# Performance work log

Measured on AMD Instinct MI355X. Metric: run time of the kernel, lower is better.

The kernel has to match this reference:

```python
import jax, jax.numpy as jnp
import numpy as np

DIN = 1024
DIM = 1024
NUM_HEADS = 16
HEAD_DIM = DIM // NUM_HEADS
SEQ_LEN = 2048
BATCH = 2


def setup_inputs() -> dict:
    key = jax.random.key(0)
    ks = jax.random.split(key, 5)
    s = 0.02
    x = jax.random.normal(ks[0], (BATCH, SEQ_LEN, DIN), dtype=jnp.float32)
    # torch nn.Linear weights are (out_features, in_features)
    wq = jax.random.normal(ks[1], (DIM, DIN), dtype=jnp.float32) * s
    wk = jax.random.normal(ks[2], (DIM, DIN), dtype=jnp.float32) * s
    wv = jax.random.normal(ks[3], (DIM, DIN), dtype=jnp.float32) * s
    wo = jax.random.normal(ks[4], (DIM, DIM), dtype=jnp.float32) * s
    return {"x": x, "wq": wq, "wk": wk, "wv": wv, "wo": wo}


def reference(x, wq, wk, wv, wo):
    bs, seq_len, _ = x.shape
    # project and split heads: [b, h, s, d]
    def split(z):
        return z.reshape(bs, seq_len, NUM_HEADS, HEAD_DIM).transpose(0, 2, 1, 3)
    q = split(x @ wq.T)
    k = split(x @ wk.T)
    v = split(x @ wv.T)
    # raw scores, causal mask applied BEFORE the 1/sqrt(d) scaling (as in source;
    # -inf is invariant to positive scaling so math matches standard causal attn)
    att = jnp.einsum('bhqd,bhkd->bhqk', q, k)
    causal = jnp.triu(jnp.ones((seq_len, seq_len), dtype=bool), k=1)
    att = jnp.where(causal, -jnp.inf, att)
    att = jax.nn.softmax(att / jnp.sqrt(jnp.float32(HEAD_DIM)), axis=-1)
    ctx = jnp.einsum('bhqk,bhkd->bhqd', att, v)
    ctx = ctx.transpose(0, 2, 1, 3).reshape(bs, seq_len, DIM)
    return ctx @ wo.T
```

## Files before the change

kernel.cpp:

```cpp
#include <hip/hip_runtime.h>
#include <stdint.h>

#define DIN 1024
#define DIMM 1024
#define NH 16
#define HD 64
#define SEQ 2048
#define BATCH 2
#define MTOT (BATCH*SEQ)
#define SCALE 0.125f

typedef __bf16 bf16;
typedef __bf16 bf16x8 __attribute__((ext_vector_type(8)));
typedef __bf16 bf16x4 __attribute__((ext_vector_type(4)));
typedef float f32x4 __attribute__((ext_vector_type(4)));

__device__ __forceinline__ void async16(bf16* lds, const bf16* g) {
  __builtin_amdgcn_global_load_lds(
      (const __attribute__((address_space(1))) void*)g,
      (__attribute__((address_space(3))) void*)lds, 16, 0, 0);
}

#define WAIT_VM(n)  asm volatile("s_waitcnt vmcnt(" #n ")" ::: "memory")
#define BARRIER()   asm volatile("s_barrier" ::: "memory")

__global__ __launch_bounds__(256) void convert_all(const float* __restrict__ x,
                                                   const float* __restrict__ wq,
                                                   const float* __restrict__ wk,
                                                   const float* __restrict__ wv,
                                                   const float* __restrict__ wo,
                                                   bf16* __restrict__ xb,
                                                   bf16* __restrict__ Wb) {
  const int t = blockIdx.x * 256 + threadIdx.x;
#pragma unroll
  for (int i = 0; i < 4; ++i) {
    const int c = t + i * 262144;
    const float* src;
    bf16* dst;
    if (c < 524288) {
      src = x + (size_t)c * 8;
      dst = xb + (size_t)c * 8;
    } else {
      const int cw = c - 524288;
      const int w = cw >> 17;
      const int off = (cw & 131071) * 8;
      const float* wp = (w == 0) ? wq : (w == 1) ? wk : (w == 2) ? wv : wo;
      src = wp + off;
      dst = Wb + (size_t)w * 1048576 + off;
    }
    f32x4 a = *(const f32x4*)src;
    f32x4 b = *(const f32x4*)(src + 4);
    bf16x8 r;
    r[0] = (bf16)a[0]; r[1] = (bf16)a[1]; r[2] = (bf16)a[2]; r[3] = (bf16)a[3];
    r[4] = (bf16)b[0]; r[5] = (bf16)b[1]; r[6] = (bf16)b[2]; r[7] = (bf16)b[3];
    *(bf16x8*)dst = r;
  }
}

__global__ __launch_bounds__(256, 2) void qkv_gemm(const bf16* __restrict__ A,
                                                   const bf16* __restrict__ B,
                                                   bf16* __restrict__ Q,
                                                   bf16* __restrict__ Kb,
                                                   bf16* __restrict__ Vt) {
  __shared__ bf16 As0[128 * 64];
  __shared__ bf16 As1[128 * 64];
  __shared__ bf16 Bs0[192 * 64];
  __shared__ bf16 Bs1[192 * 64];
  const int tid  = threadIdx.x;
  const int lane = tid & 63;
  const int wave = tid >> 6;
  const int lrow = lane & 15;
  const int quad = lane >> 4;
  const int wrow = wave >> 1;
  const int wcol = wave & 1;
  const int lin  = blockIdx.x;
  const int xcd  = lin & 7;
  const int idx  = lin >> 3;
  const int nbase = (xcd * 2 + (idx & 1)) * 192;
  const int mbase = (idx >> 1) * 128;

  const int srow = tid >> 3;
  const int sdst = srow * 64 + (tid & 7) * 8;
  const int sx   = ((tid & 7) ^ (srow & 7)) * 8;

  const bf16* ap = A + (size_t)(mbase + srow) * DIN + sx;
  const bf16* bp = B + (size_t)(nbase + srow) * DIN + sx;

  f32x4 acc[4][6] = {};

#define QKV_STAGE(Asb, Bsb)                                          \
  do {                                                               \
    _Pragma("unroll")                                                \
    for (int i = 0; i < 4; ++i)                                      \
      async16(&Asb[sdst + i * 2048], ap + (size_t)i * 32 * DIN);     \
    _Pragma("unroll")                                                \
    for (int i = 0; i < 6; ++i)                                      \
      async16(&Bsb[sdst + i * 2048], bp + (size_t)i * 32 * DIN);     \
  } while (0)

#define QKV_COMPUTE(Asb, Bsb)                                        \
  do {                                                               \
    __builtin_amdgcn_s_setprio(1);                                   \
    _Pragma("unroll")                                                \
    for (int h = 0; h < 2; ++h) {                                    \
      const int cx = ((h * 4 + quad) ^ (lrow & 7)) * 8;              \
      bf16x8 af[4], bfr[6];                                          \
      _Pragma("unroll")                                              \
      for (int i = 0; i < 4; ++i)                                    \
        af[i] = *(const bf16x8*)&Asb[(wrow * 64 + i * 16 + lrow) * 64 + cx]; \
      _Pragma("unroll")                                              \
      for (int j = 0; j < 6; ++j)                                    \
        bfr[j] = *(const bf16x8*)&Bsb[(wcol * 96 + j * 16 + lrow) * 64 + cx]; \
      _Pragma("unroll")                                              \
      for (int i = 0; i < 4; ++i)                                    \
        _Pragma("unroll")                                            \
        for (int j = 0; j < 6; ++j)                                  \
          acc[i][j] = __builtin_amdgcn_mfma_f32_16x16x32_bf16(af[i], bfr[j], acc[i][j], 0, 0, 0); \
    }                                                                \
    __builtin_amdgcn_s_setprio(0);                                   \
  } while (0)

  QKV_STAGE(As0, Bs0);
  WAIT_VM(0);
  BARRIER();

#pragma unroll 1
  for (int t = 0; t < 16; t += 2) {
    ap += 64; bp += 64;
    QKV_STAGE(As1, Bs1);
    WAIT_VM(10);
    BARRIER();
    QKV_COMPUTE(As0, Bs0);
    BARRIER();
    if (t + 2 < 16) {
      ap += 64; bp += 64;
      QKV_STAGE(As0, Bs0);
      WAIT_VM(10);
    } else {
      WAIT_VM(0);
    }
    BARRIER();
    QKV_COMPUTE(As1, Bs1);
    BARRIER();
  }

#undef QKV_STAGE
#undef QKV_COMPUTE

  const float C1 = 0.18033688f;
#pragma unroll
  for (int mt = 0; mt < 4; ++mt) {
    const int m0 = mbase + wrow * 64 + mt * 16 + quad * 4;
#pragma unroll
    for (int nt = 0; nt < 6; ++nt) {
      const int n16 = nbase + wcol * 96 + nt * 16;
      const int n = n16 + lrow;
      if (n16 < 1024) {
#pragma unroll
        for (int rr = 0; rr < 4; ++rr)
          Q[(size_t)(m0 + rr) * 1024 + n] = (bf16)(acc[mt][nt][rr] * C1);
      } else if (n16 < 2048) {
#pragma unroll
        for (int rr = 0; rr < 4; ++rr)
          Kb[(size_t)(m0 + rr) * 1024 + (n - 1024)] = (bf16)acc[mt][nt][rr];
      } else {
        const int nn = n - 2048;
        const int row = ((m0 >> 11) * 16 + (nn >> 6)) * 64 + (nn & 63);
        const int kb  = m0 & 2047;
        const int colp = (kb & ~31) | (quad * 8) | ((mt & 1) * 4);
        bf16x4 ov;
#pragma unroll
        for (int rr = 0; rr < 4; ++rr) ov[rr] = (bf16)acc[mt][nt][rr];
        *(bf16x4*)&Vt[(size_t)row * SEQ + colp] = ov;
      }
    }
  }
}

__global__ __launch_bounds__(256, 2) void proj_gemm(const bf16* __restrict__ A,
                                                    const bf16* __restrict__ B,
                                                    float* __restrict__ C) {
  __shared__ bf16 As0[128 * 64];
  __shared__ bf16 As1[128 * 64];
  __shared__ bf16 Bs0[64 * 64];
  __shared__ bf16 Bs1[64 * 64];
  const int tid  = threadIdx.x;
  const int lane = tid & 63;
  const int wave = tid >> 6;
  const int lrow = lane & 15;
  const int quad = lane >> 4;
  const int wr = (wave >> 1) * 64;
  const int wc = (wave & 1) * 32;
  const int lin = blockIdx.x;
  const int xcd = lin & 7;
  const int idx = lin >> 3;
  const int nbase = (xcd * 2 + (idx & 1)) * 64;
  const int mbase = (idx >> 1) * 128;
  const int srow = tid >> 3;
  const int sdst = srow * 64 + (tid & 7) * 8;
  const int sx   = ((tid & 7) ^ (srow & 7)) * 8;

  const bf16* ap = A + (size_t)(mbase + srow) * DIMM + sx;
  const bf16* bp = B + (size_t)(nbase + srow) * DIMM + sx;

  f32x4 acc[4][2] = {};

#define PRJ_STAGE(Asb, Bsb)                                          \
  do {                                                               \
    _Pragma("unroll")                                                \
    for (int i = 0; i < 4; ++i)                                      \
      async16(&Asb[sdst + i * 2048], ap + (size_t)i * 32 * DIMM);    \
    _Pragma("unroll")                                                \
    for (int i = 0; i < 2; ++i)                                      \
      async16(&Bsb[sdst + i * 2048], bp + (size_t)i * 32 * DIMM);    \
  } while (0)

#define PRJ_COMPUTE(Asb, Bsb)                                        \
  do {                                                               \
    __builtin_amdgcn_s_setprio(1);                                   \
    _Pragma("unroll")                                                \
    for (int h = 0; h < 2; ++h) {                                    \
      const int cx = ((h * 4 + quad) ^ (lrow & 7)) * 8;              \
      bf16x8 af[4], bfr[2];                                          \
      _Pragma("unroll")                                              \
      for (int i = 0; i < 4; ++i)                                    \
        af[i] = *(const bf16x8*)&Asb[(wr + i * 16 + lrow) * 64 + cx]; \
      _Pragma("unroll")                                              \
      for (int i = 0; i < 2; ++i)                                    \
        bfr[i] = *(const bf16x8*)&Bsb[(wc + i * 16 + lrow) * 64 + cx]; \
      _Pragma("unroll")                                              \
      for (int mt = 0; mt < 4; ++mt)                                 \
        _Pragma("unroll")                                            \
        for (int nt = 0; nt < 2; ++nt)                               \
          acc[mt][nt] = __builtin_amdgcn_mfma_f32_16x16x32_bf16(af[mt], bfr[nt], acc[mt][nt], 0, 0, 0); \
    }                                                                \
    __builtin_amdgcn_s_setprio(0);                                   \
  } while (0)

  PRJ_STAGE(As0, Bs0);
  WAIT_VM(0);
  BARRIER();

#pragma unroll 1
  for (int t = 0; t < 16; t += 2) {
    ap += 64; bp += 64;
    PRJ_STAGE(As1, Bs1);
    WAIT_VM(6);
    BARRIER();
    PRJ_COMPUTE(As0, Bs0);
    BARRIER();
    if (t + 2 < 16) {
      ap += 64; bp += 64;
      PRJ_STAGE(As0, Bs0);
      WAIT_VM(6);
    } else {
      WAIT_VM(0);
    }
    BARRIER();
    PRJ_COMPUTE(As1, Bs1);
    BARRIER();
  }

#undef PRJ_STAGE
#undef PRJ_COMPUTE

#pragma unroll
  for (int mt = 0; mt < 4; ++mt) {
    const int m0 = mbase + wr + mt * 16 + quad * 4;
#pragma unroll
    for (int nt = 0; nt < 2; ++nt) {
      const int n = nbase + wc + nt * 16 + lrow;
#pragma unroll
      for (int rr = 0; rr < 4; ++rr)
        C[(size_t)(m0 + rr) * 1024 + n] = acc[mt][nt][rr];
    }
  }
}

__global__ __launch_bounds__(256, 2) void attn(const bf16* __restrict__ Q,
                                               const bf16* __restrict__ K,
                                               const bf16* __restrict__ Vt,
                                               bf16* __restrict__ O) {
  __shared__ bf16 Ks[2][128 * 64];
  __shared__ bf16 Vts[2][128 * 64];
  const int tid  = threadIdx.x;
  const int wave = tid >> 6;
  const int lane = tid & 63;
  const int lrow = lane & 15;
  const int quad = lane >> 4;
  const int lin  = blockIdx.x;
  const int bh   = lin & 31;
  const int pp   = lin >> 5;
  const int b = bh >> 4;
  const int h = bh & 15;

  const bf16* Qh  = Q  + (size_t)(b * SEQ) * DIMM + h * HD;
  const bf16* Kh  = K  + (size_t)(b * SEQ) * DIMM + h * HD;
  const bf16* Vth = Vt + (size_t)bh * 64 * SEQ;

  const int srow = tid >> 3;
  const int sdst = srow * 64 + (tid & 7) * 8;
  const int sx   = ((tid & 7) ^ (srow & 7)) * 8;
  const int cx0 = ((0 + quad) ^ (lrow & 7)) * 8;
  const int cx1 = ((4 + quad) ^ (lrow & 7)) * 8;

#define ATT_STAGE(buf, kg, vg)                                        \
  do {                                                                \
    _Pragma("unroll")                                                 \
    for (int i = 0; i < 4; ++i)                                       \
      async16(&Ks[buf][sdst + i * 2048], kg + (size_t)i * 32 * DIMM); \
    async16(&Vts[buf][sdst],        vg);                              \
    async16(&Vts[buf][sdst + 2048], vg + (size_t)32 * SEQ);           \
    async16(&Vts[buf][sdst + 4096], vg + 64);                         \
    async16(&Vts[buf][sdst + 6144], vg + (size_t)32 * SEQ + 64);      \
  } while (0)

#pragma unroll 1
  for (int seg = 0; seg < 2; ++seg) {
    const int qi = seg ? pp : (31 - pp);
    const int qw = qi * 64 + wave * 16;
    const int nt = (qi + 2) >> 1;

    bf16x8 qf0 = *(const bf16x8*)&Qh[(size_t)(qw + lrow) * DIMM + quad * 8];
    bf16x8 qf1 = *(const bf16x8*)&Qh[(size_t)(qw + lrow) * DIMM + 32 + quad * 8];

    const bf16* kg = Kh + (size_t)srow * DIMM + sx;
    const bf16* vg = Vth + (size_t)srow * SEQ + sx;

    ATT_STAGE(0, kg, vg);
    __syncthreads();

    f32x4 lacc = {};
    f32x4 o_acc[4] = {};
    int cur = 0;

    for (int kt = 0; kt < nt; ++kt) {
      if (kt + 1 < nt) {
        kg += 128 * DIMM; vg += 128;
        const int nb = cur ^ 1;
        ATT_STAGE(nb, kg, vg);
      }
      const bf16* Kc = Ks[cur];
      const bf16* Vc = Vts[cur];
      f32x4 s[8];
#pragma unroll
      for (int gg = 0; gg < 8; ++gg) {
        s[gg] = f32x4{};
        bf16x8 kf0 = *(const bf16x8*)&Kc[(gg * 16 + lrow) * 64 + cx0];
        bf16x8 kf1 = *(const bf16x8*)&Kc[(gg * 16 + lrow) * 64 + cx1];
        s[gg] = __builtin_amdgcn_mfma_f32_16x16x32_bf16(kf0, qf0, s[gg], 0, 0, 0);
        s[gg] = __builtin_amdgcn_mfma_f32_16x16x32_bf16(kf1, qf1, s[gg], 0, 0, 0);
      }
      if (kt == nt - 1) {
        const int qrow = qw + lrow;
        const int kbase = kt * 128;
#pragma unroll
        for (int gg = 0; gg < 8; ++gg)
#pragma unroll
          for (int r = 0; r < 4; ++r)
            s[gg][r] = (kbase + gg * 16 + quad * 4 + r > qrow) ? -1e30f : s[gg][r];
      }
      bf16x8 pf0, pf1, pf2, pf3;
#pragma unroll
      for (int gg = 0; gg < 8; ++gg)
#pragma unroll
        for (int r = 0; r < 4; ++r) {
          const float p = __builtin_amdgcn_exp2f(s[gg][r]);
          lacc[r] += p;
          if      (gg < 2) pf0[(gg & 1) * 4 + r] = (bf16)p;
          else if (gg < 4) pf1[(gg & 1) * 4 + r] = (bf16)p;
          else if (gg < 6) pf2[(gg & 1) * 4 + r] = (bf16)p;
          else             pf3[(gg & 1) * 4 + r] = (bf16)p;
        }
#pragma unroll
      for (int dt = 0; dt < 4; ++dt) {
        const bf16* Vr0 = &Vc[(dt * 16 + lrow) * 64];
        const bf16* Vr1 = &Vc[4096 + (dt * 16 + lrow) * 64];
        bf16x8 vA = *(const bf16x8*)&Vr0[cx0];
        bf16x8 vB = *(const bf16x8*)&Vr0[cx1];
        bf16x8 vC = *(const bf16x8*)&Vr1[cx0];
        bf16x8 vD = *(const bf16x8*)&Vr1[cx1];
        o_acc[dt] = __builtin_amdgcn_mfma_f32_16x16x32_bf16(vA, pf0, o_acc[dt], 0, 0, 0);
        o_acc[dt] = __builtin_amdgcn_mfma_f32_16x16x32_bf16(vB, pf1, o_acc[dt], 0, 0, 0);
        o_acc[dt] = __builtin_amdgcn_mfma_f32_16x16x32_bf16(vC, pf2, o_acc[dt], 0, 0, 0);
        o_acc[dt] = __builtin_amdgcn_mfma_f32_16x16x32_bf16(vD, pf3, o_acc[dt], 0, 0, 0);
      }
      __syncthreads();
      cur ^= 1;
    }

    float lsum = (lacc[0] + lacc[1]) + (lacc[2] + lacc[3]);
    lsum += __shfl_xor(lsum, 16);
    lsum += __shfl_xor(lsum, 32);
    const float rl = __builtin_amdgcn_rcpf(lsum);
    bf16* Ob = O + (size_t)(b * SEQ + qw + lrow) * DIMM + h * HD;
#pragma unroll
    for (int dt = 0; dt < 4; ++dt) {
      bf16x4 ov;
#pragma unroll
      for (int r = 0; r < 4; ++r)
        ov[r] = (bf16)(o_acc[dt][r] * rl);
      *(bf16x4*)&Ob[dt * 16 + quad * 4] = ov;
    }
  }
#undef ATT_STAGE
}

extern "C" void kernel_launch(void* const* d_in, const int* in_sizes, int n_in,
                              void* d_out, int out_size, void* d_ws, size_t ws_size,
                              hipStream_t stream) {
  const float* x  = (const float*)d_in[0];
  const float* wq = (const float*)d_in[1];
  const float* wk = (const float*)d_in[2];
  const float* wv = (const float*)d_in[3];
  const float* wo = (const float*)d_in[4];

  const size_t M4 = (size_t)MTOT * DIMM;
  bf16* xb  = (bf16*)d_ws;
  bf16* Wb  = xb + M4;
  bf16* Q   = Wb + M4;
  bf16* Kb  = Q + M4;
  bf16* Vt  = Kb + M4;
  bf16* CTX = xb;
  float* out = (float*)d_out;

  convert_all<<<dim3(1024), dim3(256), 0, stream>>>(x, wq, wk, wv, wo, xb, Wb);
  qkv_gemm<<<dim3(512), dim3(256), 0, stream>>>(xb, Wb, Q, Kb, Vt);
  attn<<<dim3(512), dim3(256), 0, stream>>>(Q, Kb, Vt, CTX);
  proj_gemm<<<dim3(512), dim3(256), 0, stream>>>(CTX, Wb + 3 * 1048576, out);
}
```

Before: 157.6 us.

## Double attention query tile per block so each wave processes two query sub-tiles

The attention kernel now gives each block a 128-row query tile, with each wave handling two 16-row sub-tiles. Every K/V tile staged in LDS is therefore reused across twice as many queries, halving K/V global traffic and LDS fragment loads per query row. Grid size halves to 256 blocks and launch bounds drop to one block per CU to make room for the doubled registers. The risk is lower occupancy, fewer blocks than a GPU with many CUs can keep busy, and coarser causal load balancing across blocks.

```diff
diff --git a/kernel.cpp b/kernel.cpp
--- a/kernel.cpp
+++ b/kernel.cpp
@@ -277,7 +277,7 @@
   }
 }
 
-__global__ __launch_bounds__(256, 2) void attn(const bf16* __restrict__ Q,
+__global__ __launch_bounds__(256, 1) void attn(const bf16* __restrict__ Q,
                                                const bf16* __restrict__ K,
                                                const bf16* __restrict__ Vt,
                                                bf16* __restrict__ O) {
@@ -317,12 +317,14 @@
 
 #pragma unroll 1
   for (int seg = 0; seg < 2; ++seg) {
-    const int qi = seg ? pp : (31 - pp);
-    const int qw = qi * 64 + wave * 16;
-    const int nt = (qi + 2) >> 1;
-
-    bf16x8 qf0 = *(const bf16x8*)&Qh[(size_t)(qw + lrow) * DIMM + quad * 8];
-    bf16x8 qf1 = *(const bf16x8*)&Qh[(size_t)(qw + lrow) * DIMM + 32 + quad * 8];
+    const int qi = seg ? pp : (15 - pp);
+    const int qbw = qi * 128 + wave * 32;
+    const int nt = qi + 1;
+
+    bf16x8 qf0a = *(const bf16x8*)&Qh[(size_t)(qbw + lrow) * DIMM + quad * 8];
+    bf16x8 qf1a = *(const bf16x8*)&Qh[(size_t)(qbw + lrow) * DIMM + 32 + quad * 8];
+    bf16x8 qf0b = *(const bf16x8*)&Qh[(size_t)(qbw + 16 + lrow) * DIMM + quad * 8];
+    bf16x8 qf1b = *(const bf16x8*)&Qh[(size_t)(qbw + 16 + lrow) * DIMM + 32 + quad * 8];
 
     const bf16* kg = Kh + (size_t)srow * DIMM + sx;
     const bf16* vg = Vth + (size_t)srow * SEQ + sx;
@@ -330,47 +332,54 @@
     ATT_STAGE(0, kg, vg);
     __syncthreads();
 
-    f32x4 lacc = {};
-    f32x4 o_acc[4] = {};
+    f32x4 lacca = {}, laccb = {};
+    f32x4 oa[4] = {}, ob[4] = {};
     int cur = 0;
 
     for (int kt = 0; kt < nt; ++kt) {
       if (kt + 1 < nt) {
         kg += 128 * DIMM; vg += 128;
-        const int nb = cur ^ 1;
-        ATT_STAGE(nb, kg, vg);
+        ATT_STAGE(cur ^ 1, kg, vg);
       }
       const bf16* Kc = Ks[cur];
       const bf16* Vc = Vts[cur];
-      f32x4 s[8];
+      f32x4 sa[8], sb[8];
 #pragma unroll
       for (int gg = 0; gg < 8; ++gg) {
-        s[gg] = f32x4{};
+        sa[gg] = f32x4{}; sb[gg] = f32x4{};
         bf16x8 kf0 = *(const bf16x8*)&Kc[(gg * 16 + lrow) * 64 + cx0];
         bf16x8 kf1 = *(const bf16x8*)&Kc[(gg * 16 + lrow) * 64 + cx1];
-        s[gg] = __builtin_amdgcn_mfma_f32_16x16x32_bf16(kf0, qf0, s[gg], 0, 0, 0);
-        s[gg] = __builtin_amdgcn_mfma_f32_16x16x32_bf16(kf1, qf1, s[gg], 0, 0, 0);
+        sa[gg] = __builtin_amdgcn_mfma_f32_16x16x32_bf16(kf0, qf0a, sa[gg], 0, 0, 0);
+        sa[gg] = __builtin_amdgcn_mfma_f32_16x16x32_bf16(kf1, qf1a, sa[gg], 0, 0, 0);
+        sb[gg] = __builtin_amdgcn_mfma_f32_16x16x32_bf16(kf0, qf0b, sb[gg], 0, 0, 0);
+        sb[gg] = __builtin_amdgcn_mfma_f32_16x16x32_bf16(kf1, qf1b, sb[gg], 0, 0, 0);
       }
       if (kt == nt - 1) {
-        const int qrow = qw + lrow;
         const int kbase = kt * 128;
+        const int qra = qbw + lrow;
+        const int qrb = qbw + 16 + lrow;
 #pragma unroll
         for (int gg = 0; gg < 8; ++gg)
 #pragma unroll
-          for (int r = 0; r < 4; ++r)
-            s[gg][r] = (kbase + gg * 16 + quad * 4 + r > qrow) ? -1e30f : s[gg][r];
-      }
-      bf16x8 pf0, pf1, pf2, pf3;
+          for (int r = 0; r < 4; ++r) {
+            const int kk = kbase + gg * 16 + quad * 4 + r;
+            sa[gg][r] = (kk > qra) ? -1e30f : sa[gg][r];
+            sb[gg][r] = (kk > qrb) ? -1e30f : sb[gg][r];
+          }
+      }
+      bf16x8 pfa0, pfa1, pfa2, pfa3, pfb0, pfb1, pfb2, pfb3;
 #pragma unroll
       for (int gg = 0; gg < 8; ++gg)
 #pragma unroll
         for (int r = 0; r < 4; ++r) {
-          const float p = __builtin_amdgcn_exp2f(s[gg][r]);
-          lacc[r] += p;
-          if      (gg < 2) pf0[(gg & 1) * 4 + r] = (bf16)p;
-          else if (gg < 4) pf1[(gg & 1) * 4 + r] = (bf16)p;
-          else if (gg < 6) pf2[(gg & 1) * 4 + r] = (bf16)p;
-          else             pf3[(gg & 1) * 4 + r] = (bf16)p;
+          const float pa = __builtin_amdgcn_exp2f(sa[gg][r]);
+          const float pb = __builtin_amdgcn_exp2f(sb[gg][r]);
+          lacca[r] += pa;
+          laccb[r] += pb;
+          if      (gg < 2) { pfa0[(gg & 1) * 4 + r] = (bf16)pa; pfb0[(gg & 1) * 4 + r] = (bf16)pb; }
+          else if (gg < 4) { pfa1[(gg & 1) * 4 + r] = (bf16)pa; pfb1[(gg & 1) * 4 + r] = (bf16)pb; }
+          else if (gg < 6) { pfa2[(gg & 1) * 4 + r] = (bf16)pa; pfb2[(gg & 1) * 4 + r] = (bf16)pb; }
+          else             { pfa3[(gg & 1) * 4 + r] = (bf16)pa; pfb3[(gg & 1) * 4 + r] = (bf16)pb; }
         }
 #pragma unroll
       for (int dt = 0; dt < 4; ++dt) {
@@ -380,27 +389,39 @@
         bf16x8 vB = *(const bf16x8*)&Vr0[cx1];
         bf16x8 vC = *(const bf16x8*)&Vr1[cx0];
         bf16x8 vD = *(const bf16x8*)&Vr1[cx1];
-        o_acc[dt] = __builtin_amdgcn_mfma_f32_16x16x32_bf16(vA, pf0, o_acc[dt], 0, 0, 0);
-        o_acc[dt] = __builtin_amdgcn_mfma_f32_16x16x32_bf16(vB, pf1, o_acc[dt], 0, 0, 0);
-        o_acc[dt] = __builtin_amdgcn_mfma_f32_16x16x32_bf16(vC, pf2, o_acc[dt], 0, 0, 0);
-        o_acc[dt] = __builtin_amdgcn_mfma_f32_16x16x32_bf16(vD, pf3, o_acc[dt], 0, 0, 0);
+        oa[dt] = __builtin_amdgcn_mfma_f32_16x16x32_bf16(vA, pfa0, oa[dt], 0, 0, 0);
+        oa[dt] = __builtin_amdgcn_mfma_f32_16x16x32_bf16(vB, pfa1, oa[dt], 0, 0, 0);
+        oa[dt] = __builtin_amdgcn_mfma_f32_16x16x32_bf16(vC, pfa2, oa[dt], 0, 0, 0);
+        oa[dt] = __builtin_amdgcn_mfma_f32_16x16x32_bf16(vD, pfa3, oa[dt], 0, 0, 0);
+        ob[dt] = __builtin_amdgcn_mfma_f32_16x16x32_bf16(vA, pfb0, ob[dt], 0, 0, 0);
+        ob[dt] = __builtin_amdgcn_mfma_f32_16x16x32_bf16(vB, pfb1, ob[dt], 0, 0, 0);
+        ob[dt] = __builtin_amdgcn_mfma_f32_16x16x32_bf16(vC, pfb2, ob[dt], 0, 0, 0);
+        ob[dt] = __builtin_amdgcn_mfma_f32_16x16x32_bf16(vD, pfb3, ob[dt], 0, 0, 0);
       }
       __syncthreads();
       cur ^= 1;
     }
 
-    float lsum = (lacc[0] + lacc[1]) + (lacc[2] + lacc[3]);
-    lsum += __shfl_xor(lsum, 16);
-    lsum += __shfl_xor(lsum, 32);
-    const float rl = __builtin_amdgcn_rcpf(lsum);
-    bf16* Ob = O + (size_t)(b * SEQ + qw + lrow) * DIMM + h * HD;
+    float lsa = (lacca[0] + lacca[1]) + (lacca[2] + lacca[3]);
+    lsa += __shfl_xor(lsa, 16);
+    lsa += __shfl_xor(lsa, 32);
+    const float rla = __builtin_amdgcn_rcpf(lsa);
+    float lsb = (laccb[0] + laccb[1]) + (laccb[2] + laccb[3]);
+    lsb += __shfl_xor(lsb, 16);
+    lsb += __shfl_xor(lsb, 32);
+    const float rlb = __builtin_amdgcn_rcpf(lsb);
+    bf16* Oa = O + (size_t)(b * SEQ + qbw + lrow) * DIMM + h * HD;
+    bf16* Ob = O + (size_t)(b * SEQ + qbw + 16 + lrow) * DIMM + h * HD;
 #pragma unroll
     for (int dt = 0; dt < 4; ++dt) {
-      bf16x4 ov;
-#pragma unroll
-      for (int r = 0; r < 4; ++r)
-        ov[r] = (bf16)(o_acc[dt][r] * rl);
-      *(bf16x4*)&Ob[dt * 16 + quad * 4] = ov;
+      bf16x4 ova, ovb;
+#pragma unroll
+      for (int r = 0; r < 4; ++r) {
+        ova[r] = (bf16)(oa[dt][r] * rla);
+        ovb[r] = (bf16)(ob[dt][r] * rlb);
+      }
+      *(bf16x4*)&Oa[dt * 16 + quad * 4] = ova;
+      *(bf16x4*)&Ob[dt * 16 + quad * 4] = ovb;
     }
   }
 #undef ATT_STAGE
@@ -426,6 +447,6 @@
 
   convert_all<<<dim3(1024), dim3(256), 0, stream>>>(x, wq, wk, wv, wo, xb, Wb);
   qkv_gemm<<<dim3(512), dim3(256), 0, stream>>>(xb, Wb, Q, Kb, Vt);
-  attn<<<dim3(512), dim3(256), 0, stream>>>(Q, Kb, Vt, CTX);
+  attn<<<dim3(256), dim3(256), 0, stream>>>(Q, Kb, Vt, CTX);
   proj_gemm<<<dim3(512), dim3(256), 0, stream>>>(CTX, Wb + 3 * 1048576, out);
 }
```

After: 167.4 us. +6.2%, slower.

## Split attention key tile across waves and reduce partial outputs through LDS

Applied to the files above, without the earlier changes.

Each wave previously owned 16 query rows and processed all 128 keys of a tile. Now each wave owns 32 keys of the tile and computes scores for all 64 query rows, so each wave loads fewer K/V fragments from LDS and reuses one V fragment across four MFMAs. Partial softmax sums and partial output accumulators are reduced across waves through LDS at the end of each segment, reusing the K/V buffers. This adds a cross-wave reduction, extra barriers and more accumulator registers (16 o_acc vectors), which may hurt occupancy.

```diff
diff --git a/kernel.cpp b/kernel.cpp
--- a/kernel.cpp
+++ b/kernel.cpp
@@ -283,6 +283,7 @@
                                                bf16* __restrict__ O) {
   __shared__ bf16 Ks[2][128 * 64];
   __shared__ bf16 Vts[2][128 * 64];
+  __shared__ float Lred[4][64];
   const int tid  = threadIdx.x;
   const int wave = tid >> 6;
   const int lane = tid & 63;
@@ -303,26 +304,33 @@
   const int sx   = ((tid & 7) ^ (srow & 7)) * 8;
   const int cx0 = ((0 + quad) ^ (lrow & 7)) * 8;
   const int cx1 = ((4 + quad) ^ (lrow & 7)) * 8;
-
-#define ATT_STAGE(buf, kg, vg)                                        \
-  do {                                                                \
-    _Pragma("unroll")                                                 \
-    for (int i = 0; i < 4; ++i)                                       \
-      async16(&Ks[buf][sdst + i * 2048], kg + (size_t)i * 32 * DIMM); \
-    async16(&Vts[buf][sdst],        vg);                              \
-    async16(&Vts[buf][sdst + 2048], vg + (size_t)32 * SEQ);           \
-    async16(&Vts[buf][sdst + 4096], vg + 64);                         \
-    async16(&Vts[buf][sdst + 6144], vg + (size_t)32 * SEQ + 64);      \
+  const int kwb  = wave * 32;
+  const int vsub = (wave >> 1) * 4096;
+  const int vcx  = (wave & 1) ? cx1 : cx0;
+
+#define ATT_STAGE(buf, kg_, vg_)                                       \
+  do {                                                                 \
+    _Pragma("unroll")                                                  \
+    for (int i = 0; i < 4; ++i)                                        \
+      async16(&Ks[buf][sdst + i * 2048], kg_ + (size_t)i * 32 * DIMM); \
+    async16(&Vts[buf][sdst],        vg_);                              \
+    async16(&Vts[buf][sdst + 2048], vg_ + (size_t)32 * SEQ);           \
+    async16(&Vts[buf][sdst + 4096], vg_ + 64);                         \
+    async16(&Vts[buf][sdst + 6144], vg_ + (size_t)32 * SEQ + 64);      \
   } while (0)
 
 #pragma unroll 1
   for (int seg = 0; seg < 2; ++seg) {
     const int qi = seg ? pp : (31 - pp);
-    const int qw = qi * 64 + wave * 16;
+    const int qw = qi * 64;
     const int nt = (qi + 2) >> 1;
 
-    bf16x8 qf0 = *(const bf16x8*)&Qh[(size_t)(qw + lrow) * DIMM + quad * 8];
-    bf16x8 qf1 = *(const bf16x8*)&Qh[(size_t)(qw + lrow) * DIMM + 32 + quad * 8];
+    bf16x8 qf[4][2];
+#pragma unroll
+    for (int qg = 0; qg < 4; ++qg) {
+      qf[qg][0] = *(const bf16x8*)&Qh[(size_t)(qw + qg * 16 + lrow) * DIMM + quad * 8];
+      qf[qg][1] = *(const bf16x8*)&Qh[(size_t)(qw + qg * 16 + lrow) * DIMM + 32 + quad * 8];
+    }
 
     const bf16* kg = Kh + (size_t)srow * DIMM + sx;
     const bf16* vg = Vth + (size_t)srow * SEQ + sx;
@@ -330,78 +338,100 @@
     ATT_STAGE(0, kg, vg);
     __syncthreads();
 
-    f32x4 lacc = {};
-    f32x4 o_acc[4] = {};
+    f32x4 lacc[4] = {};
+    f32x4 o_acc[4][4] = {};
     int cur = 0;
 
     for (int kt = 0; kt < nt; ++kt) {
       if (kt + 1 < nt) {
         kg += 128 * DIMM; vg += 128;
-        const int nb = cur ^ 1;
-        ATT_STAGE(nb, kg, vg);
+        ATT_STAGE(cur ^ 1, kg, vg);
       }
       const bf16* Kc = Ks[cur];
       const bf16* Vc = Vts[cur];
-      f32x4 s[8];
-#pragma unroll
-      for (int gg = 0; gg < 8; ++gg) {
-        s[gg] = f32x4{};
-        bf16x8 kf0 = *(const bf16x8*)&Kc[(gg * 16 + lrow) * 64 + cx0];
-        bf16x8 kf1 = *(const bf16x8*)&Kc[(gg * 16 + lrow) * 64 + cx1];
-        s[gg] = __builtin_amdgcn_mfma_f32_16x16x32_bf16(kf0, qf0, s[gg], 0, 0, 0);
-        s[gg] = __builtin_amdgcn_mfma_f32_16x16x32_bf16(kf1, qf1, s[gg], 0, 0, 0);
+      bf16x8 kf0a = *(const bf16x8*)&Kc[(kwb + lrow) * 64 + cx0];
+      bf16x8 kf0b = *(const bf16x8*)&Kc[(kwb + lrow) * 64 + cx1];
+      bf16x8 kf1a = *(const bf16x8*)&Kc[(kwb + 16 + lrow) * 64 + cx0];
+      bf16x8 kf1b = *(const bf16x8*)&Kc[(kwb + 16 + lrow) * 64 + cx1];
+      f32x4 s[4][2];
+#pragma unroll
+      for (int qg = 0; qg < 4; ++qg) {
+        s[qg][0] = f32x4{}; s[qg][1] = f32x4{};
+        s[qg][0] = __builtin_amdgcn_mfma_f32_16x16x32_bf16(kf0a, qf[qg][0], s[qg][0], 0, 0, 0);
+        s[qg][0] = __builtin_amdgcn_mfma_f32_16x16x32_bf16(kf0b, qf[qg][1], s[qg][0], 0, 0, 0);
+        s[qg][1] = __builtin_amdgcn_mfma_f32_16x16x32_bf16(kf1a, qf[qg][0], s[qg][1], 0, 0, 0);
+        s[qg][1] = __builtin_amdgcn_mfma_f32_16x16x32_bf16(kf1b, qf[qg][1], s[qg][1], 0, 0, 0);
       }
       if (kt == nt - 1) {
-        const int qrow = qw + lrow;
-        const int kbase = kt * 128;
-#pragma unroll
-        for (int gg = 0; gg < 8; ++gg)
-#pragma unroll
-          for (int r = 0; r < 4; ++r)
-            s[gg][r] = (kbase + gg * 16 + quad * 4 + r > qrow) ? -1e30f : s[gg][r];
-      }
-      bf16x8 pf0, pf1, pf2, pf3;
-#pragma unroll
-      for (int gg = 0; gg < 8; ++gg)
-#pragma unroll
-        for (int r = 0; r < 4; ++r) {
-          const float p = __builtin_amdgcn_exp2f(s[gg][r]);
-          lacc[r] += p;
-          if      (gg < 2) pf0[(gg & 1) * 4 + r] = (bf16)p;
-          else if (gg < 4) pf1[(gg & 1) * 4 + r] = (bf16)p;
-          else if (gg < 6) pf2[(gg & 1) * 4 + r] = (bf16)p;
-          else             pf3[(gg & 1) * 4 + r] = (bf16)p;
+        const int kb0 = kt * 128 + kwb;
+#pragma unroll
+        for (int qg = 0; qg < 4; ++qg) {
+          const int qrow = qw + qg * 16 + lrow;
+#pragma unroll
+          for (int kg2 = 0; kg2 < 2; ++kg2)
+#pragma unroll
+            for (int r = 0; r < 4; ++r)
+              s[qg][kg2][r] = (kb0 + kg2 * 16 + quad * 4 + r > qrow) ? -1e30f : s[qg][kg2][r];
         }
+      }
+      bf16x8 pf[4];
+#pragma unroll
+      for (int qg = 0; qg < 4; ++qg)
+#pragma unroll
+        for (int kg2 = 0; kg2 < 2; ++kg2)
+#pragma unroll
+          for (int r = 0; r < 4; ++r) {
+            const float p = __builtin_amdgcn_exp2f(s[qg][kg2][r]);
+            lacc[qg][r] += p;
+            pf[qg][kg2 * 4 + r] = (bf16)p;
+          }
 #pragma unroll
       for (int dt = 0; dt < 4; ++dt) {
-        const bf16* Vr0 = &Vc[(dt * 16 + lrow) * 64];
-        const bf16* Vr1 = &Vc[4096 + (dt * 16 + lrow) * 64];
-        bf16x8 vA = *(const bf16x8*)&Vr0[cx0];
-        bf16x8 vB = *(const bf16x8*)&Vr0[cx1];
-        bf16x8 vC = *(const bf16x8*)&Vr1[cx0];
-        bf16x8 vD = *(const bf16x8*)&Vr1[cx1];
-        o_acc[dt] = __builtin_amdgcn_mfma_f32_16x16x32_bf16(vA, pf0, o_acc[dt], 0, 0, 0);
-        o_acc[dt] = __builtin_amdgcn_mfma_f32_16x16x32_bf16(vB, pf1, o_acc[dt], 0, 0, 0);
-        o_acc[dt] = __builtin_amdgcn_mfma_f32_16x16x32_bf16(vC, pf2, o_acc[dt], 0, 0, 0);
-        o_acc[dt] = __builtin_amdgcn_mfma_f32_16x16x32_bf16(vD, pf3, o_acc[dt], 0, 0, 0);
+        bf16x8 vf = *(const bf16x8*)&Vc[vsub + (dt * 16 + lrow) * 64 + vcx];
+#pragma unroll
+        for (int qg = 0; qg < 4; ++qg)
+          o_acc[dt][qg] = __builtin_amdgcn_mfma_f32_16x16x32_bf16(vf, pf[qg], o_acc[dt][qg], 0, 0, 0);
       }
       __syncthreads();
       cur ^= 1;
     }
 
-    float lsum = (lacc[0] + lacc[1]) + (lacc[2] + lacc[3]);
-    lsum += __shfl_xor(lsum, 16);
-    lsum += __shfl_xor(lsum, 32);
-    const float rl = __builtin_amdgcn_rcpf(lsum);
-    bf16* Ob = O + (size_t)(b * SEQ + qw + lrow) * DIMM + h * HD;
+#pragma unroll
+    for (int qg = 0; qg < 4; ++qg) {
+      float ls = (lacc[qg][0] + lacc[qg][1]) + (lacc[qg][2] + lacc[qg][3]);
+      ls += __shfl_xor(ls, 16);
+      ls += __shfl_xor(ls, 32);
+      if (quad == 0) Lred[wave][qg * 16 + lrow] = ls;
+    }
+    float* OLb = (wave < 2) ? ((float*)&Ks[0][0] + wave * 4096)
+                            : ((float*)&Vts[0][0] + (wave - 2) * 4096);
+#pragma unroll
+    for (int dt = 0; dt < 4; ++dt)
+#pragma unroll
+      for (int qg = 0; qg < 4; ++qg)
+        *(f32x4*)&OLb[(dt * 4 + qg) * 256 + lane * 4] = o_acc[dt][qg];
+    __syncthreads();
+    const float lt = Lred[0][wave * 16 + lrow] + Lred[1][wave * 16 + lrow]
+                   + Lred[2][wave * 16 + lrow] + Lred[3][wave * 16 + lrow];
+    const float rl = __builtin_amdgcn_rcpf(lt);
+    bf16* Ob = O + (size_t)(b * SEQ + qw + wave * 16 + lrow) * DIMM + h * HD;
 #pragma unroll
     for (int dt = 0; dt < 4; ++dt) {
+      f32x4 sum = {};
+#pragma unroll
+      for (int w2 = 0; w2 < 4; ++w2) {
+        const float* Bs2 = (w2 < 2) ? ((float*)&Ks[0][0] + w2 * 4096)
+                                    : ((float*)&Vts[0][0] + (w2 - 2) * 4096);
+        f32x4 part = *(const f32x4*)&Bs2[(dt * 4 + wave) * 256 + lane * 4];
+#pragma unroll
+        for (int r = 0; r < 4; ++r) sum[r] += part[r];
+      }
       bf16x4 ov;
 #pragma unroll
-      for (int r = 0; r < 4; ++r)
-        ov[r] = (bf16)(o_acc[dt][r] * rl);
+      for (int r = 0; r < 4; ++r) ov[r] = (bf16)(sum[r] * rl);
       *(bf16x4*)&Ob[dt * 16 + quad * 4] = ov;
     }
+    __syncthreads();
   }
 #undef ATT_STAGE
 }
```

New measurement: 161.1 us. +2.2%, slower.

## Drop attention double buffering and paired segments for higher occupancy

Applied to the files above, without the earlier changes.

The attention kernel now uses a single LDS buffer for K and V instead of two, and each block handles one query tile instead of a balanced pair (longest tiles first, 1024 blocks). Launch bounds go from 2 to 5 blocks per CU, so more resident waves can hide load latency instead of explicit prefetch. The cost is that async loads are no longer overlapped with compute inside a block, each tile waits on its load, and per-block work is now uneven.

```diff
diff --git a/kernel.cpp b/kernel.cpp
--- a/kernel.cpp
+++ b/kernel.cpp
@@ -277,12 +277,12 @@
   }
 }
 
-__global__ __launch_bounds__(256, 2) void attn(const bf16* __restrict__ Q,
+__global__ __launch_bounds__(256, 5) void attn(const bf16* __restrict__ Q,
                                                const bf16* __restrict__ K,
                                                const bf16* __restrict__ Vt,
                                                bf16* __restrict__ O) {
-  __shared__ bf16 Ks[2][128 * 64];
-  __shared__ bf16 Vts[2][128 * 64];
+  __shared__ bf16 Ks[128 * 64];
+  __shared__ bf16 Vts[128 * 64];
   const int tid  = threadIdx.x;
   const int wave = tid >> 6;
   const int lane = tid & 63;
@@ -290,9 +290,11 @@
   const int quad = lane >> 4;
   const int lin  = blockIdx.x;
   const int bh   = lin & 31;
-  const int pp   = lin >> 5;
+  const int qi   = 31 - (lin >> 5);
   const int b = bh >> 4;
   const int h = bh & 15;
+  const int qw = qi * 64 + wave * 16;
+  const int nt = (qi + 2) >> 1;
 
   const bf16* Qh  = Q  + (size_t)(b * SEQ) * DIMM + h * HD;
   const bf16* Kh  = K  + (size_t)(b * SEQ) * DIMM + h * HD;
@@ -304,106 +306,85 @@
   const int cx0 = ((0 + quad) ^ (lrow & 7)) * 8;
   const int cx1 = ((4 + quad) ^ (lrow & 7)) * 8;
 
-#define ATT_STAGE(buf, kg, vg)                                        \
-  do {                                                                \
-    _Pragma("unroll")                                                 \
-    for (int i = 0; i < 4; ++i)                                       \
-      async16(&Ks[buf][sdst + i * 2048], kg + (size_t)i * 32 * DIMM); \
-    async16(&Vts[buf][sdst],        vg);                              \
-    async16(&Vts[buf][sdst + 2048], vg + (size_t)32 * SEQ);           \
-    async16(&Vts[buf][sdst + 4096], vg + 64);                         \
-    async16(&Vts[buf][sdst + 6144], vg + (size_t)32 * SEQ + 64);      \
-  } while (0)
+  bf16x8 qf0 = *(const bf16x8*)&Qh[(size_t)(qw + lrow) * DIMM + quad * 8];
+  bf16x8 qf1 = *(const bf16x8*)&Qh[(size_t)(qw + lrow) * DIMM + 32 + quad * 8];
+
+  const bf16* kg = Kh + (size_t)srow * DIMM + sx;
+  const bf16* vg = Vth + (size_t)srow * SEQ + sx;
+
+  f32x4 lacc = {};
+  f32x4 o_acc[4] = {};
 
 #pragma unroll 1
-  for (int seg = 0; seg < 2; ++seg) {
-    const int qi = seg ? pp : (31 - pp);
-    const int qw = qi * 64 + wave * 16;
-    const int nt = (qi + 2) >> 1;
-
-    bf16x8 qf0 = *(const bf16x8*)&Qh[(size_t)(qw + lrow) * DIMM + quad * 8];
-    bf16x8 qf1 = *(const bf16x8*)&Qh[(size_t)(qw + lrow) * DIMM + 32 + quad * 8];
-
-    const bf16* kg = Kh + (size_t)srow * DIMM + sx;
-    const bf16* vg = Vth + (size_t)srow * SEQ + sx;
-
-    ATT_STAGE(0, kg, vg);
+  for (int kt = 0; kt < nt; ++kt) {
+#pragma unroll
+    for (int i = 0; i < 4; ++i)
+      async16(&Ks[sdst + i * 2048], kg + (size_t)i * 32 * DIMM);
+    async16(&Vts[sdst],        vg);
+    async16(&Vts[sdst + 2048], vg + (size_t)32 * SEQ);
+    async16(&Vts[sdst + 4096], vg + 64);
+    async16(&Vts[sdst + 6144], vg + (size_t)32 * SEQ + 64);
+    kg += 128 * DIMM; vg += 128;
     __syncthreads();
-
-    f32x4 lacc = {};
-    f32x4 o_acc[4] = {};
-    int cur = 0;
-
-    for (int kt = 0; kt < nt; ++kt) {
-      if (kt + 1 < nt) {
-        kg += 128 * DIMM; vg += 128;
-        const int nb = cur ^ 1;
-        ATT_STAGE(nb, kg, vg);
+    f32x4 s[8];
+#pragma unroll
+    for (int gg = 0; gg < 8; ++gg) {
+      s[gg] = f32x4{};
+      bf16x8 kf0 = *(const bf16x8*)&Ks[(gg * 16 + lrow) * 64 + cx0];
+      bf16x8 kf1 = *(const bf16x8*)&Ks[(gg * 16 + lrow) * 64 + cx1];
+      s[gg] = __builtin_amdgcn_mfma_f32_16x16x32_bf16(kf0, qf0, s[gg], 0, 0, 0);
+      s[gg] = __builtin_amdgcn_mfma_f32_16x16x32_bf16(kf1, qf1, s[gg], 0, 0, 0);
+    }
+    if (kt == nt - 1) {
+      const int qrow = qw + lrow;
+      const int kbase = kt * 128;
+#pragma unroll
+      for (int gg = 0; gg < 8; ++gg)
+#pragma unroll
+        for (int r = 0; r < 4; ++r)
+          s[gg][r] = (kbase + gg * 16 + quad * 4 + r > qrow) ? -1e30f : s[gg][r];
+    }
+    bf16x8 pf0, pf1, pf2, pf3;
+#pragma unroll
+    for (int gg = 0; gg < 8; ++gg)
+#pragma unroll
+      for (int r = 0; r < 4; ++r) {
+        const float p = __builtin_amdgcn_exp2f(s[gg][r]);
+        lacc[r] += p;
+        if      (gg < 2) pf0[(gg & 1) * 4 + r] = (bf16)p;
+        else if (gg < 4) pf1[(gg & 1) * 4 + r] = (bf16)p;
+        else if (gg < 6) pf2[(gg & 1) * 4 + r] = (bf16)p;
+        else             pf3[(gg & 1) * 4 + r] = (bf16)p;
       }
-      const bf16* Kc = Ks[cur];
-      const bf16* Vc = Vts[cur];
-      f32x4 s[8];
-#pragma unroll
-      for (int gg = 0; gg < 8; ++gg) {
-        s[gg] = f32x4{};
-        bf16x8 kf0 = *(const bf16x8*)&Kc[(gg * 16 + lrow) * 64 + cx0];
-        bf16x8 kf1 = *(const bf16x8*)&Kc[(gg * 16 + lrow) * 64 + cx1];
-        s[gg] = __builtin_amdgcn_mfma_f32_16x16x32_bf16(kf0, qf0, s[gg], 0, 0, 0);
-        s[gg] = __builtin_amdgcn_mfma_f32_16x16x32_bf16(kf1, qf1, s[gg], 0, 0, 0);
-      }
-      if (kt == nt - 1) {
-        const int qrow = qw + lrow;
-        const int kbase = kt * 128;
-#pragma unroll
-        for (int gg = 0; gg < 8; ++gg)
-#pragma unroll
-          for (int r = 0; r < 4; ++r)
-            s[gg][r] = (kbase + gg * 16 + quad * 4 + r > qrow) ? -1e30f : s[gg][r];
-      }
-      bf16x8 pf0, pf1, pf2, pf3;
-#pragma unroll
-      for (int gg = 0; gg < 8; ++gg)
-#pragma unroll
-        for (int r = 0; r < 4; ++r) {
-          const float p = __builtin_amdgcn_exp2f(s[gg][r]);
-          lacc[r] += p;
-          if      (gg < 2) pf0[(gg & 1) * 4 + r] = (bf16)p;
-          else if (gg < 4) pf1[(gg & 1) * 4 + r] = (bf16)p;
-          else if (gg < 6) pf2[(gg & 1) * 4 + r] = (bf16)p;
-          else             pf3[(gg & 1) * 4 + r] = (bf16)p;
-        }
-#pragma unroll
-      for (int dt = 0; dt < 4; ++dt) {
-        const bf16* Vr0 = &Vc[(dt * 16 + lrow) * 64];
-        const bf16* Vr1 = &Vc[4096 + (dt * 16 + lrow) * 64];
-        bf16x8 vA = *(const bf16x8*)&Vr0[cx0];
-        bf16x8 vB = *(const bf16x8*)&Vr0[cx1];
-        bf16x8 vC = *(const bf16x8*)&Vr1[cx0];
-        bf16x8 vD = *(const bf16x8*)&Vr1[cx1];
-        o_acc[dt] = __builtin_amdgcn_mfma_f32_16x16x32_bf16(vA, pf0, o_acc[dt], 0, 0, 0);
-        o_acc[dt] = __builtin_amdgcn_mfma_f32_16x16x32_bf16(vB, pf1, o_acc[dt], 0, 0, 0);
-        o_acc[dt] = __builtin_amdgcn_mfma_f32_16x16x32_bf16(vC, pf2, o_acc[dt], 0, 0, 0);
-        o_acc[dt] = __builtin_amdgcn_mfma_f32_16x16x32_bf16(vD, pf3, o_acc[dt], 0, 0, 0);
-      }
-      __syncthreads();
-      cur ^= 1;
-    }
-
-    float lsum = (lacc[0] + lacc[1]) + (lacc[2] + lacc[3]);
-    lsum += __shfl_xor(lsum, 16);
-    lsum += __shfl_xor(lsum, 32);
-    const float rl = __builtin_amdgcn_rcpf(lsum);
-    bf16* Ob = O + (size_t)(b * SEQ + qw + lrow) * DIMM + h * HD;
 #pragma unroll
     for (int dt = 0; dt < 4; ++dt) {
-      bf16x4 ov;
-#pragma unroll
-      for (int r = 0; r < 4; ++r)
-        ov[r] = (bf16)(o_acc[dt][r] * rl);
-      *(bf16x4*)&Ob[dt * 16 + quad * 4] = ov;
-    }
-  }
-#undef ATT_STAGE
+      const bf16* Vr0 = &Vts[(dt * 16 + lrow) * 64];
+      const bf16* Vr1 = &Vts[4096 + (dt * 16 + lrow) * 64];
+      bf16x8 vA = *(const bf16x8*)&Vr0[cx0];
+      bf16x8 vB = *(const bf16x8*)&Vr0[cx1];
+      bf16x8 vC = *(const bf16x8*)&Vr1[cx0];
+      bf16x8 vD = *(const bf16x8*)&Vr1[cx1];
+      o_acc[dt] = __builtin_amdgcn_mfma_f32_16x16x32_bf16(vA, pf0, o_acc[dt], 0, 0, 0);
+      o_acc[dt] = __builtin_amdgcn_mfma_f32_16x16x32_bf16(vB, pf1, o_acc[dt], 0, 0, 0);
+      o_acc[dt] = __builtin_amdgcn_mfma_f32_16x16x32_bf16(vC, pf2, o_acc[dt], 0, 0, 0);
+      o_acc[dt] = __builtin_amdgcn_mfma_f32_16x16x32_bf16(vD, pf3, o_acc[dt], 0, 0, 0);
+    }
+    __syncthreads();
+  }
+
+  float lsum = (lacc[0] + lacc[1]) + (lacc[2] + lacc[3]);
+  lsum += __shfl_xor(lsum, 16);
+  lsum += __shfl_xor(lsum, 32);
+  const float rl = __builtin_amdgcn_rcpf(lsum);
+  bf16* Ob = O + (size_t)(b * SEQ + qw + lrow) * DIMM + h * HD;
+#pragma unroll
+  for (int dt = 0; dt < 4; ++dt) {
+    bf16x4 ov;
+#pragma unroll
+    for (int r = 0; r < 4; ++r)
+      ov[r] = (bf16)(o_acc[dt][r] * rl);
+    *(bf16x4*)&Ob[dt * 16 + quad * 4] = ov;
+  }
 }
 
 extern "C" void kernel_launch(void* const* d_in, const int* in_sizes, int n_in,
@@ -426,6 +407,6 @@
 
   convert_all<<<dim3(1024), dim3(256), 0, stream>>>(x, wq, wk, wv, wo, xb, Wb);
   qkv_gemm<<<dim3(512), dim3(256), 0, stream>>>(xb, Wb, Q, Kb, Vt);
-  attn<<<dim3(512), dim3(256), 0, stream>>>(Q, Kb, Vt, CTX);
+  attn<<<dim3(1024), dim3(256), 0, stream>>>(Q, Kb, Vt, CTX);
   proj_gemm<<<dim3(512), dim3(256), 0, stream>>>(CTX, Wb + 3 * 1048576, out);
 }
```

Result: no change. 157.1 us (-0.3%).
